# Optimization experiments

Hardware: AMD Instinct MI355X
Metric: run time of the kernel (lower is better)

Reference implementation:

```python
import jax, jax.numpy as jnp
import numpy as np

B, T, D = 2, 2048, 2048
H, HD = 16, 128
HHD = HD // 2
SCALE = 1.0 / np.sqrt(HHD).astype(np.float32)


def setup_inputs() -> dict:
    key = jax.random.key(0)
    ks = jax.random.split(key, 6)
    s = 1.0 / np.sqrt(D).astype(np.float32)
    return {
        "x": jax.random.normal(ks[0], (B, T, D), jnp.float32),
        "Wq": jax.random.normal(ks[1], (D, H * HD), jnp.float32) * s,
        "Wk": jax.random.normal(ks[2], (D, H * HD), jnp.float32) * s,
        "Wv": jax.random.normal(ks[3], (D, H * HD), jnp.float32) * s,
        "Wo": jax.random.normal(ks[4], (H * HD, D), jnp.float32) * s,
        "lambda_init": jnp.full((H,), -0.2, jnp.float32),
    }


def reference(x, Wq, Wk, Wv, Wo, lambda_init):
    b, t, d = x.shape
    # projections -> (B, H, T, HD)
    q = (x @ Wq).reshape(b, t, H, HD).transpose(0, 2, 1, 3)
    k = (x @ Wk).reshape(b, t, H, HD).transpose(0, 2, 1, 3)
    v = (x @ Wv).reshape(b, t, H, HD).transpose(0, 2, 1, 3)
    q1, q2 = q[..., :HHD], q[..., HHD:]
    k1, k2 = k[..., :HHD], k[..., HHD:]
    scores1 = jnp.einsum('bhtc,bhsc->bhts', q1, k1) * SCALE
    scores2 = jnp.einsum('bhtc,bhsc->bhts', q2, k2) * SCALE
    causal = jnp.tril(jnp.ones((t, t), bool))  # (T, T)
    neg_inf = jnp.float32(-jnp.inf)
    scores1 = jnp.where(causal[None, None], scores1, neg_inf)
    scores2 = jnp.where(causal[None, None], scores2, neg_inf)
    attn1 = jax.nn.softmax(scores1, axis=-1)
    attn2 = jax.nn.softmax(scores2, axis=-1)
    lam = jax.nn.sigmoid(lambda_init)[None, :, None, None]
    diff_attn = attn1 - lam * attn2
    out = jnp.einsum('bhts,bhsd->bhtd', diff_attn, v)
    out = out.transpose(0, 2, 1, 3).reshape(b, t, H * HD)
    return out @ Wo
```

## Files before the change

### kernel.cpp

```cpp
#include <hip/hip_runtime.h>
#include <cstdint>
#include <cstddef>


typedef unsigned short u16;
typedef __bf16 bf16x8 __attribute__((ext_vector_type(8)));
typedef float f32x4 __attribute__((ext_vector_type(4)));

#define LOG2E 1.44269504088896340736f
#define KS 0.18033688011112042f
#define CB 11.541560327111707f

__device__ __forceinline__ u16 f2bu(float f) {
  unsigned int x = __float_as_uint(f);
  x += 0x7fffu + ((x >> 16) & 1u);
  return (u16)(x >> 16);
}

__device__ __forceinline__ void stage16(const void* g, void* lds_uniform, int lane) {
#if defined(__has_builtin) && __has_builtin(__builtin_amdgcn_global_load_lds)
  (void)lane;
  __builtin_amdgcn_global_load_lds(
      (__attribute__((address_space(1))) void*)(g),
      (__attribute__((address_space(3))) void*)(lds_uniform), 16, 0, 0);
#else
  *(uint4*)((char*)lds_uniform + lane * 16) = *(const uint4*)g;
#endif
}

__device__ __forceinline__ void stageK(const char* g, char* lds_u) {
#if defined(__has_builtin) && __has_builtin(__builtin_amdgcn_global_load_lds)
  __builtin_amdgcn_global_load_lds(
      (__attribute__((address_space(1))) void*)g,
      (__attribute__((address_space(3))) void*)lds_u, 16, 0, 0);
  __builtin_amdgcn_global_load_lds(
      (__attribute__((address_space(1))) void*)(g + (size_t)128 * 4096),
      (__attribute__((address_space(3))) void*)(lds_u + 8192), 16, 0, 0);
#endif
}

__device__ __forceinline__ void stage2(const char* g, void* lds_u) {
#if defined(__has_builtin) && __has_builtin(__builtin_amdgcn_global_load_lds)
  __builtin_amdgcn_global_load_lds(
      (__attribute__((address_space(1))) void*)g,
      (__attribute__((address_space(3))) void*)lds_u, 16, 0, 0);
  __builtin_amdgcn_global_load_lds(
      (__attribute__((address_space(1))) void*)(g + 64),
      (__attribute__((address_space(3))) void*)((char*)lds_u + 8192), 16, 0, 0);
#endif
}

__global__ void f32_to_bf16_k(const float* __restrict__ in, u16* __restrict__ out, int n4) {
  int i = blockIdx.x * blockDim.x + threadIdx.x;
  if (i < n4) {
    float4 v = ((const float4*)in)[i];
    ushort4 u;
    u.x = f2bu(v.x); u.y = f2bu(v.y); u.z = f2bu(v.z); u.w = f2bu(v.w);
    ((ushort4*)out)[i] = u;
  }
}

__global__ void transpose_f32_bf16(const float* __restrict__ in, u16* __restrict__ out,
                                   int R, int C) {
  __shared__ u16 tile[32][33];
  const int tx = threadIdx.x & 31, ty = threadIdx.x >> 5;
  const int c0 = blockIdx.x * 32, r0 = blockIdx.y * 32;
#pragma unroll
  for (int i = 0; i < 32; i += 8)
    tile[ty + i][tx] = f2bu(in[(size_t)(r0 + ty + i) * C + c0 + tx]);
  __syncthreads();
#pragma unroll
  for (int i = 0; i < 32; i += 8)
    out[(size_t)(c0 + ty + i) * R + r0 + tx] = tile[tx][ty + i];
}

__global__ void transpose3_f32_bf16(const float* __restrict__ W0,
                                    const float* __restrict__ W1,
                                    const float* __restrict__ W2,
                                    u16* __restrict__ out) {
  __shared__ u16 tile[32][33];
  const float* in = blockIdx.z == 0 ? W0 : (blockIdx.z == 1 ? W1 : W2);
  u16* o = out + (size_t)blockIdx.z * 2048 * 2048;
  const int tx = threadIdx.x & 31, ty = threadIdx.x >> 5;
  const int c0 = blockIdx.x * 32, r0 = blockIdx.y * 32;
#pragma unroll
  for (int i = 0; i < 32; i += 8)
    tile[ty + i][tx] = f2bu(in[(size_t)(r0 + ty + i) * 2048 + c0 + tx]);
  __syncthreads();
#pragma unroll
  for (int i = 0; i < 32; i += 8)
    o[(size_t)(c0 + ty + i) * 2048 + r0 + tx] = tile[tx][ty + i];
}

template <int MODE>
__global__ void gemm_bt(const u16* __restrict__ A, const u16* __restrict__ BT,
                        void* __restrict__ C, u16* __restrict__ C2,
                        int Mdim, int Ndim, int Kdim) {
  __shared__ __align__(16) u16 As[128 * 32];
  __shared__ __align__(16) u16 Bs[128 * 32];
  const int tid = threadIdx.x;
  const int lane = tid & 63;
  const int w = tid >> 6;
  const int wm = w & 1, wn = w >> 1;
  const int li = lane & 15, lh = lane >> 4;
  const int m0 = blockIdx.x * 128;
  const int n0 = blockIdx.y * 128;

  const f32x4 fzero = {0.f, 0.f, 0.f, 0.f};
  f32x4 acc[4][4];
#pragma unroll
  for (int i = 0; i < 4; ++i)
#pragma unroll
    for (int jj = 0; jj < 4; ++jj) acc[i][jj] = fzero;

  for (int k0 = 0; k0 < Kdim; k0 += 32) {
#pragma unroll
    for (int i = 0; i < 2; ++i) {
      const int c = i * 256 + w * 64 + lane;
      stage16(A + (size_t)(m0 + (c >> 2)) * Kdim + k0 + ((c & 3) << 3),
              (char*)As + (size_t)(i * 256 + w * 64) * 16, lane);
      stage16(BT + (size_t)(n0 + (c >> 2)) * Kdim + k0 + ((c & 3) << 3),
              (char*)Bs + (size_t)(i * 256 + w * 64) * 16, lane);
    }
    __syncthreads();

    bf16x8 af[4], bfr[4];
#pragma unroll
    for (int mt = 0; mt < 4; ++mt)
      af[mt] = *(const bf16x8*)&As[(wm * 64 + mt * 16 + li) * 32 + lh * 8];
#pragma unroll
    for (int nt = 0; nt < 4; ++nt)
      bfr[nt] = *(const bf16x8*)&Bs[(wn * 64 + nt * 16 + li) * 32 + lh * 8];
#pragma unroll
    for (int mt = 0; mt < 4; ++mt)
#pragma unroll
      for (int nt = 0; nt < 4; ++nt)
        acc[mt][nt] = __builtin_amdgcn_mfma_f32_16x16x32_bf16(af[mt], bfr[nt], acc[mt][nt], 0, 0, 0);
    __syncthreads();
  }

#pragma unroll
  for (int mt = 0; mt < 4; ++mt) {
#pragma unroll
    for (int nt = 0; nt < 4; ++nt) {
      const int mb = m0 + wm * 64 + mt * 16 + lh * 4;
      const int n = n0 + wn * 64 + nt * 16 + li;
      if (MODE == 0) {
        u16* o = (u16*)C;
#pragma unroll
        for (int r = 0; r < 4; ++r)
          o[(size_t)(mb + r) * Ndim + n] = f2bu(acc[mt][nt][r]);
      } else if (MODE == 1) {
        float* o = (float*)C;
#pragma unroll
        for (int r = 0; r < 4; ++r)
          o[(size_t)(mb + r) * Ndim + n] = acc[mt][nt][r];
      } else {
        u16* o = (u16*)C;
        const int bb = mb >> 11, t = mb & 2047;
        const int hh = n >> 7, d = n & 127;
        ushort4 u;
        u.x = f2bu(acc[mt][nt][0]);
        u.y = f2bu(acc[mt][nt][1]);
        u.z = f2bu(acc[mt][nt][2]);
        u.w = f2bu(acc[mt][nt][3]);
        *(ushort4*)&o[((size_t)((bb * 16 + hh) * 128 + d) << 11) + t] = u;
      }
    }
  }
}

template <int OMODE, int NTPX>
__global__ __launch_bounds__(512, 2)
void gemm_pipe(const u16* __restrict__ A, const u16* __restrict__ BT,
               void* __restrict__ C, u16* __restrict__ C2) {
  __shared__ __align__(16) u16 As[3][2][128][32];
  __shared__ __align__(16) u16 Bs[6][2][128][32];

  const int tid = threadIdx.x;
  const int w = tid >> 6;
  const int lane = tid & 63;
  const int wm = w >> 2;
  const int wn = w & 3;
  const int wh = wn >> 1;
  const int li = lane & 15, lh = lane >> 4;
  const int lhx8 = (lh ^ (((li >> 3) & 1) << 1)) * 8;
  const int brow = (wn & 1) * 64;

  const int bid = blockIdx.x;
  const int xcd = bid & 7;
  const int local = bid >> 3;
  const int mtile = local / NTPX;
  const int ntile = xcd * NTPX + (local % NTPX);
  const int m0 = mtile * 128, n0 = ntile * 256;

  const int o = tid << 4;
  const int osz = o ^ (((o >> 9) & 1) << 5);
  const int srow = osz >> 6;
  const int skel = (osz & 63) >> 1;
  const size_t soff = ((size_t)srow * 2048 + skel) * 2;

  const char* pA  = (const char*)A  + (size_t)m0 * 4096 + soff;
  const char* pB0 = (const char*)BT + (size_t)n0 * 4096 + soff;
  const char* pB1 = pB0 + (size_t)128 * 4096;

#define STAGE_A(SLOT)    { stage2(pA,  (char*)As + (SLOT) * 16384 + w * 1024); pA  += 128; }
#define STAGE_BODD(SLOT) { stage2(pB1, (char*)Bs + (SLOT) * 16384 + w * 1024); pB1 += 128; }
#define STAGE_BEVEN(SLOT){ stage2(pB0, (char*)Bs + (SLOT) * 16384 + w * 1024); pB0 += 128; }

  const f32x4 fzero = {0.f, 0.f, 0.f, 0.f};
  f32x4 acc[4][4];
#pragma unroll
  for (int i = 0; i < 4; ++i)
#pragma unroll
    for (int jj = 0; jj < 4; ++jj) acc[i][jj] = fzero;

  STAGE_A(0); STAGE_BEVEN(0); STAGE_BODD(1); STAGE_A(1); STAGE_BEVEN(2);
  asm volatile("s_waitcnt vmcnt(3)" ::: "memory");
  __builtin_amdgcn_s_barrier();
  asm volatile("" ::: "memory");

#define QPHASE(SA, SB2, KSI, STAGES, TAIL)                                     \
  {                                                                            \
    bf16x8 af[4], bfc[4];                                                      \
    _Pragma("unroll")                                                          \
    for (int mq = 0; mq < 4; ++mq)                                             \
      af[mq] = *(const bf16x8*)&As[(SA)][(KSI)][wm * 64 + mq * 16 + li][lhx8]; \
    _Pragma("unroll")                                                          \
    for (int nt = 0; nt < 4; ++nt)                                             \
      bfc[nt] = *(const bf16x8*)&Bs[(SB2) + wh][(KSI)][brow + nt * 16 + li][lhx8]; \
    STAGES;                                                                    \
    __builtin_amdgcn_s_barrier();                                              \
    asm volatile("" ::: "memory");                                             \
    __builtin_amdgcn_s_setprio(1);                                             \
    _Pragma("unroll")                                                          \
    for (int mq = 0; mq < 4; ++mq) {                                           \
      _Pragma("unroll")                                                        \
      for (int nt = 0; nt < 4; ++nt)                                           \
        acc[mq][nt] = __builtin_amdgcn_mfma_f32_16x16x32_bf16(                 \
            af[mq], bfc[nt], acc[mq][nt], 0, 0, 0);                            \
    }                                                                          \
    __builtin_amdgcn_s_setprio(0);                                             \
    TAIL;                                                                      \
    __builtin_amdgcn_s_barrier();                                              \
    asm volatile("" ::: "memory");                                             \
  }

#define TILE_MAIN(U)                                                           \
  QPHASE((U), 2 * (U), 0,                                                      \
         { STAGE_A(((U) + 2) % 3); STAGE_BODD((2 * (U) + 3) % 6); }, ((void)0)) \
  QPHASE((U), 2 * (U), 1, { STAGE_BEVEN((2 * (U) + 4) % 6); },                 \
         asm volatile("s_waitcnt vmcnt(2)" ::: "memory"))

  for (int t3 = 0; t3 < 10; ++t3) {
    TILE_MAIN(0)
    TILE_MAIN(1)
    TILE_MAIN(2)
  }
  QPHASE(0, 0, 0, { STAGE_BODD(3); }, ((void)0))
  QPHASE(0, 0, 1, ((void)0), asm volatile("s_waitcnt vmcnt(0)" ::: "memory"))
  QPHASE(1, 2, 0, ((void)0), ((void)0))
  QPHASE(1, 2, 1, ((void)0), ((void)0))

#undef QPHASE
#undef TILE_MAIN
#undef STAGE_A
#undef STAGE_BODD
#undef STAGE_BEVEN

  const int nB0 = (OMODE == 0 ? (n0 & 2047) : n0) + wn * 64;
  const int mB = m0 + wm * 64;
  const int proj = n0 >> 11;
#pragma unroll
  for (int mt = 0; mt < 4; ++mt) {
#pragma unroll
    for (int nt = 0; nt < 4; ++nt) {
      const int mb = mB + mt * 16 + lh * 4;
      const int n = nB0 + nt * 16 + li;
      if (OMODE == 1) {
        float* o = (float*)C;
#pragma unroll
        for (int r = 0; r < 4; ++r)
          o[(size_t)(mb + r) * 2048 + n] = acc[mt][nt][r];
      } else if (proj < 2) {
        u16* o = (u16*)C + (size_t)proj * 4096 * 2048;
#pragma unroll
        for (int r = 0; r < 4; ++r)
          o[(size_t)(mb + r) * 2048 + n] = f2bu(acc[mt][nt][r]);
      } else {
        const int bb = mb >> 11, t = mb & 2047;
        const int hh = n >> 7, d = n & 127;
        ushort4 u;
        u.x = f2bu(acc[mt][nt][0]);
        u.y = f2bu(acc[mt][nt][1]);
        u.z = f2bu(acc[mt][nt][2]);
        u.w = f2bu(acc[mt][nt][3]);
        *(ushort4*)&C2[((size_t)((bb * 16 + hh) * 128 + d) << 11) + t] = u;
      }
    }
  }
}

__global__ __launch_bounds__(512, 4)
void gemm_qkv2(const u16* __restrict__ A, const u16* __restrict__ BT,
               u16* __restrict__ C, u16* __restrict__ C2) {
  __shared__ __align__(16) u16 As[3][128][32];
  __shared__ __align__(16) u16 Bs[3][256][32];

  const int tid = threadIdx.x;
  const int lane = tid & 63;
  const int w = tid >> 6;
  const int wm = w >> 2;
  const int wn = w & 3;
  const int li = lane & 15, lh = lane >> 4;
  const int lhx8 = (lh ^ (((li >> 3) & 1) << 1)) * 8;

  const int bid = blockIdx.x;
  const int xcd = bid & 7;
  const int local = bid >> 3;
  const int mtile = local / 3;
  const int ntile = xcd * 3 + (local % 3);
  const int m0 = mtile * 128, n0 = ntile * 256;

  const int o = tid << 4;
  const int osz = o ^ (((o >> 9) & 1) << 5);
  const int srow = osz >> 6;
  const int skel = (osz & 63) >> 1;
  const size_t soff = ((size_t)srow * 2048 + skel) * 2;

  const char* pA = (const char*)A  + (size_t)m0 * 4096 + soff;
  const char* pB = (const char*)BT + (size_t)n0 * 4096 + soff;

#define STA(SLOT) { stage16(pA, (char*)As + (SLOT) * 8192 + w * 1024, lane); pA += 64; }
#define STB(SLOT) { stageK(pB, (char*)Bs + (SLOT) * 16384 + w * 1024); pB += 64; }

  const f32x4 fzero = {0.f, 0.f, 0.f, 0.f};
  f32x4 acc[4][4];
#pragma unroll
  for (int i = 0; i < 4; ++i)
#pragma unroll
    for (int jj = 0; jj < 4; ++jj) acc[i][jj] = fzero;

  STA(0); STB(0); STA(1); STB(1);
  asm volatile("s_waitcnt vmcnt(3)" ::: "memory");
  __builtin_amdgcn_s_barrier();
  asm volatile("" ::: "memory");

#define QP2(SLOT, STAGES, TAIL)                                                \
  {                                                                            \
    bf16x8 af[4], bfc[4];                                                      \
    _Pragma("unroll")                                                          \
    for (int mq = 0; mq < 4; ++mq)                                             \
      af[mq] = *(const bf16x8*)&As[(SLOT)][wm * 64 + mq * 16 + li][lhx8];      \
    _Pragma("unroll")                                                          \
    for (int nt = 0; nt < 4; ++nt)                                             \
      bfc[nt] = *(const bf16x8*)&Bs[(SLOT)][wn * 64 + nt * 16 + li][lhx8];     \
    STAGES;                                                                    \
    __builtin_amdgcn_s_barrier();                                              \
    asm volatile("" ::: "memory");                                             \
    __builtin_amdgcn_s_setprio(1);                                             \
    _Pragma("unroll")                                                          \
    for (int mq = 0; mq < 4; ++mq) {                                           \
      _Pragma("unroll")                                                        \
      for (int nt = 0; nt < 4; ++nt)                                           \
        acc[mq][nt] = __builtin_amdgcn_mfma_f32_16x16x32_bf16(                 \
            af[mq], bfc[nt], acc[mq][nt], 0, 0, 0);                            \
    }                                                                          \
    __builtin_amdgcn_s_setprio(0);                                             \
    TAIL;                                                                      \
    __builtin_amdgcn_s_barrier();                                              \
    asm volatile("" ::: "memory");                                             \
  }

#define VM3 asm volatile("s_waitcnt vmcnt(3)" ::: "memory")

  for (int t3 = 0; t3 < 20; ++t3) {
    QP2(0, { STA(2); STB(2); }, VM3);
    QP2(1, { STA(0); STB(0); }, VM3);
    QP2(2, { STA(1); STB(1); }, VM3);
  }
  QP2(0, { STA(2); STB(2); }, VM3);
  QP2(1, { STA(0); STB(0); }, VM3);
  QP2(2, ((void)0), asm volatile("s_waitcnt vmcnt(0)" ::: "memory"));
  QP2(0, ((void)0), ((void)0));

#undef QP2
#undef VM3
#undef STA
#undef STB

  const int proj = n0 >> 11;
  const int nB = (n0 & 2047) + wn * 64;
  const int mB = m0 + wm * 64;
#pragma unroll
  for (int mt = 0; mt < 4; ++mt) {
#pragma unroll
    for (int nt = 0; nt < 4; ++nt) {
      const int mb = mB + mt * 16 + lh * 4;
      const int n = nB + nt * 16 + li;
      if (proj < 2) {
        u16* o = C + (size_t)proj * 4096 * 2048;
#pragma unroll
        for (int r = 0; r < 4; ++r)
          o[(size_t)(mb + r) * 2048 + n] = f2bu(acc[mt][nt][r]);
      } else {
        const int bb = mb >> 11, t = mb & 2047;
        const int hh = n >> 7, d = n & 127;
        ushort4 u;
        u.x = f2bu(acc[mt][nt][0]);
        u.y = f2bu(acc[mt][nt][1]);
        u.z = f2bu(acc[mt][nt][2]);
        u.w = f2bu(acc[mt][nt][3]);
        *(ushort4*)&C2[((size_t)((bb * 16 + hh) * 128 + d) << 11) + t] = u;
      }
    }
  }
}

__device__ __forceinline__ void stage_kv(const u16* __restrict__ kbase,
                                         const u16* __restrict__ vbase, int j,
                                         u16* ksBuf, u16* vsBuf, int w, int lane) {
  const int kst_r = lane >> 4, kst_c = lane & 15;
  const int vst_r = lane >> 3, vst_c = lane & 7;
#pragma unroll
  for (int i = 0; i < 4; ++i) {
    const int t = w * 4 + i;
    const int srow = t * 4 + kst_r;
    const int scb = kst_c ^ (srow & 7);
    stage16(kbase + (size_t)(j * 64 + srow) * 2048 + scb * 8,
            (char*)ksBuf + t * 1024, lane);
    const int drow = t * 8 + vst_r;
    const int dcb = vst_c ^ (drow & 7);
    stage16(vbase + (size_t)drow * 2048 + j * 64 + dcb * 8,
            (char*)vsBuf + t * 1024, lane);
  }
}

__global__ __launch_bounds__(256, 2)
void diff_attn(const u16* __restrict__ Q, const u16* __restrict__ K,
               const u16* __restrict__ VT, const float* __restrict__ lamin,
               u16* __restrict__ AO) {
  __shared__ __align__(16) u16 Ks[2][64 * 128];
  __shared__ __align__(16) u16 Vs[2][128 * 64];
  __shared__ __align__(16) u16 Ps1[64 * 64];
  __shared__ __align__(16) u16 Ps2[64 * 64];

  const int tid = threadIdx.x, lane = tid & 63, w = tid >> 6;
  const int li = lane & 15, lh = lane >> 4;
  const int bh = blockIdx.x & 31, pair = blockIdx.x >> 5;
  const int b = bh >> 4, h = bh & 15;

  const float lam = 1.f / (1.f + exp2f(-lamin[h] * LOG2E));
  const u16* kbase = K + ((size_t)(b * 2048)) * 2048 + h * 128;
  const u16* vbase = VT + ((size_t)(b * 16 + h) << 18);
  const f32x4 fzero = {0.f, 0.f, 0.f, 0.f};

  for (int phase = 0; phase < 2; ++phase) {
    const int it = phase ? 31 - pair : pair;
    const int t0 = it * 64;

    bf16x8 qf[4];
    {
      const u16* qp = Q + (size_t)(b * 2048 + t0 + w * 16 + li) * 2048 + h * 128 + lh * 8;
#pragma unroll
      for (int kk = 0; kk < 4; ++kk) qf[kk] = *(const bf16x8*)(qp + kk * 32);
    }

    f32x4 o1[8], o2[8];
#pragma unroll
    for (int i = 0; i < 8; ++i) { o1[i] = fzero; o2[i] = fzero; }
    float l1p[4] = {0.f, 0.f, 0.f, 0.f};
    float l2p[4] = {0.f, 0.f, 0.f, 0.f};

    if (phase) __syncthreads();
    stage_kv(kbase, vbase, 0, Ks[0], Vs[0], w, lane);

    for (int j = 0; j <= it; ++j) {
      const int cur = j & 1;
      __syncthreads();
      if (j < it)
        stage_kv(kbase, vbase, j + 1, Ks[cur ^ 1], Vs[cur ^ 1], w, lane);

      const u16* __restrict__ ks = Ks[cur];
      const u16* __restrict__ vs = Vs[cur];
      const bool diag = (j == it);

#pragma unroll
      for (int nt = 0; nt < 4; ++nt) {
        const int srow = nt * 16 + li;
        const int sw = li & 7;
        bf16x8 b0 = *(const bf16x8*)&ks[srow * 128 + ((0 + lh) ^ sw) * 8];
        bf16x8 b1 = *(const bf16x8*)&ks[srow * 128 + ((4 + lh) ^ sw) * 8];
        bf16x8 b2 = *(const bf16x8*)&ks[srow * 128 + ((8 + lh) ^ sw) * 8];
        bf16x8 b3 = *(const bf16x8*)&ks[srow * 128 + ((12 + lh) ^ sw) * 8];
        f32x4 s1 = fzero, s2 = fzero;
        s1 = __builtin_amdgcn_mfma_f32_16x16x32_bf16(qf[0], b0, s1, 0, 0, 0);
        s1 = __builtin_amdgcn_mfma_f32_16x16x32_bf16(qf[1], b1, s1, 0, 0, 0);
        s2 = __builtin_amdgcn_mfma_f32_16x16x32_bf16(qf[2], b2, s2, 0, 0, 0);
        s2 = __builtin_amdgcn_mfma_f32_16x16x32_bf16(qf[3], b3, s2, 0, 0, 0);

        const int cb = nt * 2 + (li >> 3);
        const int sg = j * 64 + nt * 16 + li;
#pragma unroll
        for (int r = 0; r < 4; ++r) {
          const int row = w * 16 + lh * 4 + r;
          float p1, p2;
          if (diag && sg > t0 + row) {
            p1 = 0.f; p2 = 0.f;
          } else {
            p1 = exp2f(fmaf(s1[r], KS, -CB));
            p2 = exp2f(fmaf(s2[r], KS, -CB));
          }
          l1p[r] += p1; l2p[r] += p2;
          const int idx = row * 64 + ((cb ^ (row & 7)) << 3) + (li & 7);
          Ps1[idx] = f2bu(p1);
          Ps2[idx] = f2bu(p2);
        }
      }

#pragma unroll
      for (int kss = 0; kss < 2; ++kss) {
        const int arow = w * 16 + li;
        const int jb = ((kss * 4 + lh) ^ (li & 7)) * 8;
        bf16x8 a1f = *(const bf16x8*)&Ps1[arow * 64 + jb];
        bf16x8 a2f = *(const bf16x8*)&Ps2[arow * 64 + jb];
#pragma unroll
        for (int nt = 0; nt < 8; ++nt) {
          const int d = nt * 16 + li;
          bf16x8 vf = *(const bf16x8*)&vs[d * 64 + ((kss * 4 + lh) ^ (li & 7)) * 8];
          o1[nt] = __builtin_amdgcn_mfma_f32_16x16x32_bf16(a1f, vf, o1[nt], 0, 0, 0);
          o2[nt] = __builtin_amdgcn_mfma_f32_16x16x32_bf16(a2f, vf, o2[nt], 0, 0, 0);
        }
      }
    }

#pragma unroll
    for (int r = 0; r < 4; ++r) {
#pragma unroll
      for (int off = 1; off < 16; off <<= 1) {
        l1p[r] += __shfl_xor(l1p[r], off);
        l2p[r] += __shfl_xor(l2p[r], off);
      }
    }

#pragma unroll
    for (int r = 0; r < 4; ++r) {
      const float inv1 = 1.f / l1p[r];
      const float inv2 = lam / l2p[r];
      u16* orow = AO + (size_t)(b * 2048 + t0 + w * 16 + lh * 4 + r) * 2048 + h * 128 + li;
#pragma unroll
      for (int nt = 0; nt < 8; ++nt)
        orow[nt * 16] = f2bu(o1[nt][r] * inv1 - o2[nt][r] * inv2);
    }
  }
}

extern "C" void kernel_launch(void* const* d_in, const int* in_sizes, int n_in,
                              void* d_out, int out_size, void* d_ws, size_t ws_size,
                              hipStream_t stream) {
  const float* x   = (const float*)d_in[0];
  const float* Wq  = (const float*)d_in[1];
  const float* Wk  = (const float*)d_in[2];
  const float* Wv  = (const float*)d_in[3];
  const float* Wo  = (const float*)d_in[4];
  const float* lam = (const float*)d_in[5];
  float* out = (float*)d_out;

  const size_t MB = 1ull << 20;
  char* ws = (char*)d_ws;
  u16* qb = (u16*)d_out;
  u16* kb = qb + (size_t)4096 * 2048;

  if (ws_size >= 56 * MB) {
    u16* xb = (u16*)(ws);
    u16* wT = (u16*)(ws + 16 * MB);
    u16* vt = (u16*)(ws + 40 * MB);
    u16* ao = xb;

    f32_to_bf16_k<<<8192, 256, 0, stream>>>(x, xb, 2097152);
    transpose3_f32_bf16<<<dim3(64, 64, 3), 256, 0, stream>>>(Wq, Wk, Wv, wT);
    gemm_qkv2<<<dim3(768), 512, 0, stream>>>(xb, wT, qb, vt);

    diff_attn<<<dim3(512), 256, 0, stream>>>(qb, kb, vt, lam, ao);

    transpose_f32_bf16<<<dim3(64, 64), 256, 0, stream>>>(Wo, wT, 2048, 2048);
    gemm_pipe<1, 1><<<dim3(256), 512, 0, stream>>>(ao, wT, out, nullptr);
  } else {
    u16* xb = (u16*)(ws);
    u16* wT = (u16*)(ws + 16 * MB);
    u16* vt = (u16*)(ws + 24 * MB);
    u16* ao = xb;

    f32_to_bf16_k<<<8192, 256, 0, stream>>>(x, xb, 2097152);
    transpose_f32_bf16<<<dim3(64, 64), 256, 0, stream>>>(Wq, wT, 2048, 2048);
    gemm_bt<0><<<dim3(32, 16), 256, 0, stream>>>(xb, wT, qb, nullptr, 4096, 2048, 2048);
    transpose_f32_bf16<<<dim3(64, 64), 256, 0, stream>>>(Wk, wT, 2048, 2048);
    gemm_bt<0><<<dim3(32, 16), 256, 0, stream>>>(xb, wT, kb, nullptr, 4096, 2048, 2048);
    transpose_f32_bf16<<<dim3(64, 64), 256, 0, stream>>>(Wv, wT, 2048, 2048);
    gemm_bt<2><<<dim3(32, 16), 256, 0, stream>>>(xb, wT, vt, nullptr, 4096, 2048, 2048);

    diff_attn<<<dim3(512), 256, 0, stream>>>(qb, kb, vt, lam, ao);

    transpose_f32_bf16<<<dim3(64, 64), 256, 0, stream>>>(Wo, wT, 2048, 2048);
    gemm_bt<1><<<dim3(32, 16), 256, 0, stream>>>(ao, wT, out, nullptr, 4096, 2048, 2048);
  }
}
```

Baseline: 390.1 us.

## Fuse x cast with QKV weight transposes and double-buffer QKV GEMM

Merges the x fp32-to-bf16 cast and the three weight transposes into a single launch, removing one kernel launch and its tail. The QKV GEMM moves from a triple-buffered LDS pipeline to a double-buffered one with vmcnt(0) waits, raising launch bounds to allow more resident blocks per CU. The aim is higher occupancy, traded against less prefetch depth, so global-load latency may become exposed.

```diff
diff --git a/kernel.cpp b/kernel.cpp
--- a/kernel.cpp
+++ b/kernel.cpp
@@ -74,22 +74,36 @@
     out[(size_t)(c0 + ty + i) * R + r0 + tx] = tile[tx][ty + i];
 }
 
-__global__ void transpose3_f32_bf16(const float* __restrict__ W0,
-                                    const float* __restrict__ W1,
-                                    const float* __restrict__ W2,
-                                    u16* __restrict__ out) {
+__global__ void prep_qkv(const float* __restrict__ x,
+                         const float* __restrict__ Wq,
+                         const float* __restrict__ Wk,
+                         const float* __restrict__ Wv,
+                         u16* __restrict__ xb, u16* __restrict__ wT) {
   __shared__ u16 tile[32][33];
-  const float* in = blockIdx.z == 0 ? W0 : (blockIdx.z == 1 ? W1 : W2);
-  u16* o = out + (size_t)blockIdx.z * 2048 * 2048;
-  const int tx = threadIdx.x & 31, ty = threadIdx.x >> 5;
-  const int c0 = blockIdx.x * 32, r0 = blockIdx.y * 32;
-#pragma unroll
-  for (int i = 0; i < 32; i += 8)
-    tile[ty + i][tx] = f2bu(in[(size_t)(r0 + ty + i) * 2048 + c0 + tx]);
-  __syncthreads();
-#pragma unroll
-  for (int i = 0; i < 32; i += 8)
-    o[(size_t)(c0 + ty + i) * 2048 + r0 + tx] = tile[tx][ty + i];
+  const int bid = blockIdx.x;
+  if (bid < 8192) {
+    const int i = bid * 256 + threadIdx.x;
+    float4 v = ((const float4*)x)[i];
+    ushort4 u;
+    u.x = f2bu(v.x); u.y = f2bu(v.y); u.z = f2bu(v.z); u.w = f2bu(v.w);
+    ((ushort4*)xb)[i] = u;
+  } else {
+    const int tb = bid - 8192;
+    const int z = tb >> 12;
+    const int xy = tb & 4095;
+    const int bx = xy & 63, by = xy >> 6;
+    const float* in = z == 0 ? Wq : (z == 1 ? Wk : Wv);
+    u16* o = wT + (size_t)z * 2048 * 2048;
+    const int tx = threadIdx.x & 31, ty = threadIdx.x >> 5;
+    const int c0 = bx * 32, r0 = by * 32;
+#pragma unroll
+    for (int i = 0; i < 32; i += 8)
+      tile[ty + i][tx] = f2bu(in[(size_t)(r0 + ty + i) * 2048 + c0 + tx]);
+    __syncthreads();
+#pragma unroll
+    for (int i = 0; i < 32; i += 8)
+      o[(size_t)(c0 + ty + i) * 2048 + r0 + tx] = tile[tx][ty + i];
+  }
 }
 
 template <int MODE>
@@ -301,11 +315,11 @@
   }
 }
 
-__global__ __launch_bounds__(512, 4)
-void gemm_qkv2(const u16* __restrict__ A, const u16* __restrict__ BT,
+__global__ __launch_bounds__(512, 6)
+void gemm_qkv3(const u16* __restrict__ A, const u16* __restrict__ BT,
                u16* __restrict__ C, u16* __restrict__ C2) {
-  __shared__ __align__(16) u16 As[3][128][32];
-  __shared__ __align__(16) u16 Bs[3][256][32];
+  __shared__ __align__(16) u16 As[2][128][32];
+  __shared__ __align__(16) u16 Bs[2][256][32];
 
   const int tid = threadIdx.x;
   const int lane = tid & 63;
@@ -341,12 +355,12 @@
 #pragma unroll
     for (int jj = 0; jj < 4; ++jj) acc[i][jj] = fzero;
 
-  STA(0); STB(0); STA(1); STB(1);
-  asm volatile("s_waitcnt vmcnt(3)" ::: "memory");
+  STA(0); STB(0);
+  asm volatile("s_waitcnt vmcnt(0)" ::: "memory");
   __builtin_amdgcn_s_barrier();
   asm volatile("" ::: "memory");
 
-#define QP2(SLOT, STAGES, TAIL)                                                \
+#define QP3(SLOT, STAGES, TAIL)                                                \
   {                                                                            \
     bf16x8 af[4], bfc[4];                                                      \
     _Pragma("unroll")                                                          \
@@ -372,20 +386,17 @@
     asm volatile("" ::: "memory");                                             \
   }
 
-#define VM3 asm volatile("s_waitcnt vmcnt(3)" ::: "memory")
-
-  for (int t3 = 0; t3 < 20; ++t3) {
-    QP2(0, { STA(2); STB(2); }, VM3);
-    QP2(1, { STA(0); STB(0); }, VM3);
-    QP2(2, { STA(1); STB(1); }, VM3);
-  }
-  QP2(0, { STA(2); STB(2); }, VM3);
-  QP2(1, { STA(0); STB(0); }, VM3);
-  QP2(2, ((void)0), asm volatile("s_waitcnt vmcnt(0)" ::: "memory"));
-  QP2(0, ((void)0), ((void)0));
-
-#undef QP2
-#undef VM3
+#define VM0 asm volatile("s_waitcnt vmcnt(0)" ::: "memory")
+
+  for (int t2 = 0; t2 < 31; ++t2) {
+    QP3(0, { STA(1); STB(1); }, VM0);
+    QP3(1, { STA(0); STB(0); }, VM0);
+  }
+  QP3(0, { STA(1); STB(1); }, VM0);
+  QP3(1, ((void)0), ((void)0));
+
+#undef QP3
+#undef VM0
 #undef STA
 #undef STB
 
@@ -577,9 +588,8 @@
     u16* vt = (u16*)(ws + 40 * MB);
     u16* ao = xb;
 
-    f32_to_bf16_k<<<8192, 256, 0, stream>>>(x, xb, 2097152);
-    transpose3_f32_bf16<<<dim3(64, 64, 3), 256, 0, stream>>>(Wq, Wk, Wv, wT);
-    gemm_qkv2<<<dim3(768), 512, 0, stream>>>(xb, wT, qb, vt);
+    prep_qkv<<<dim3(20480), 256, 0, stream>>>(x, Wq, Wk, Wv, xb, wT);
+    gemm_qkv3<<<dim3(768), 512, 0, stream>>>(xb, wT, qb, vt);
 
     diff_attn<<<dim3(512), 256, 0, stream>>>(qb, kb, vt, lam, ao);
 
```

Measured after the change: 1.277 ms. 227% more time.
